# Kernel tuning notes

Hardware: AMD Instinct MI355X
Metric: run time of the kernel (lower is better)

## Reference

```python
import jax, jax.numpy as jnp
import numpy as np

B, T, D, E = 4, 2048, 1024, 8


def setup_inputs() -> dict:
    key = jax.random.key(0)
    ks = jax.random.split(key, 8)
    scale_g = float(np.sqrt(2.0 / (D + E)))  # xavier_uniform-ish scale for W_g
    scale_w = float(1.0 / np.sqrt(D))
    return {
        "x": jax.random.normal(ks[0], (B, T, D), dtype=jnp.float32),
        "noise": jax.random.normal(ks[1], (B, T, E), dtype=jnp.float32),  # the N(0,1) sample in Gating.forward
        "W_g": jax.random.normal(ks[2], (D, E), dtype=jnp.float32) * scale_g,
        "W_noise": jax.random.normal(ks[3], (D, E), dtype=jnp.float32),
        "W1": jax.random.normal(ks[4], (E, D, D), dtype=jnp.float32) * scale_w,
        "b1": jnp.zeros((E, D), dtype=jnp.float32),
        "W2": jax.random.normal(ks[5], (E, D, D), dtype=jnp.float32) * scale_w,
        "b2": jnp.zeros((E, D), dtype=jnp.float32),
        "k": 2,
    }


def _gates(x, noise, W_g, W_noise, k):
    # h = x@W_g + N(0,1) + softplus(x@W_noise)   (note: noise added, not scaled)
    h = jnp.einsum("btd,de->bte", x, W_g) + noise + jax.nn.softplus(
        jnp.einsum("btd,de->bte", x, W_noise)
    )
    kth = jax.lax.top_k(h, k)[0][..., -1:]           # kth largest per token
    h_masked = jnp.where(h >= kth, h, -jnp.inf)       # keepTopK (ties kept, as in torch)
    return jax.nn.softmax(h_masked, axis=-1)          # [B,T,E]


def reference(x, noise, W_g, W_noise, W1, b1, W2, b2, k):
    gates = _gates(x, noise, W_g, W_noise, k)
    # Dense loop over experts (faithful to original): every expert FFN on all tokens.
    # hidden: [E,B,T,D]
    hidden = jax.nn.relu(jnp.einsum("btd,edh->ebth", x, W1) + b1[:, None, None, :])
    expert_out = jnp.einsum("ebth,eho->ebto", hidden, W2) + b2[:, None, None, :]
    # mask-weighted combine: sum_e expert_out_e * gates[...,e]
    return jnp.einsum("ebtd,bte->btd", expert_out, gates)
```

## Files before the change

### kernel.cpp

```cpp
#include <hip/hip_runtime.h>
#include <hip/hip_bf16.h>

#define BTOK 8192
#define DDIM 1024
#define NEXP 8

typedef unsigned short u16;
typedef unsigned int u32;
typedef __attribute__((ext_vector_type(8))) short short8;
typedef __attribute__((ext_vector_type(4))) float f32x4;

constexpr int BM = 256, BN = 256, BK = 64;
constexpr int SLOTCAP = 3072;
constexpr int NT = DDIM / BK;

__device__ __forceinline__ u16 f2bf(float f){
  __hip_bfloat16 h = __float2bfloat16(f);
  return *reinterpret_cast<u16*>(&h);
}
__device__ __forceinline__ float bf2f(u16 v){
  return __uint_as_float(((u32)v) << 16);
}
__device__ __forceinline__ void gll16(const u16* gsrc, u16* ldst){
  __builtin_amdgcn_global_load_lds((const __attribute__((address_space(1))) void*)gsrc,
                                   (__attribute__((address_space(3))) void*)ldst,
                                   16, 0, 0);
}

#define GTOK 16
__global__ __launch_bounds__(512) void gating_score_kernel(
    const float* __restrict__ x, const float* __restrict__ noise,
    const float* __restrict__ Wg, const float* __restrict__ Wn,
    float* __restrict__ h_out, u16* __restrict__ xb)
{
  __shared__ float lw[2][NEXP][4][260];
  const int tid = threadIdx.x;

  for (int i = tid; i < 2*DDIM*NEXP; i += 512){
    const int mat = i >> 13;
    const int r   = i & 8191;
    const int d = r >> 3, ee = r & 7;
    const float* W = mat ? Wn : Wg;
    lw[mat][ee][d >> 8][d & 255] = W[r];
  }
  __syncthreads();

  const int q   = tid & 3;
  const int e   = (tid >> 2) & 7;
  const int tok = tid >> 5;
  const int t   = blockIdx.x * GTOK + tok;

  const float4* x4 = reinterpret_cast<const float4*>(x + (size_t)t*DDIM + q*256);
  const float4* g4 = reinterpret_cast<const float4*>(&lw[0][e][q][0]);
  const float4* n4 = reinterpret_cast<const float4*>(&lw[1][e][q][0]);
  ushort4* xb4 = reinterpret_cast<ushort4*>(xb + (size_t)t*DDIM + q*256);
  float agx=0.f, agz=0.f, anx=0.f, anz=0.f;
  #pragma unroll 8
  for (int j = 0; j < 64; ++j){
    const float4 xv = x4[j];
    const float4 wg = g4[j];
    const float4 wn = n4[j];
    agx = fmaf(xv.x,wg.x, fmaf(xv.y,wg.y, agx));
    agz = fmaf(xv.z,wg.z, fmaf(xv.w,wg.w, agz));
    anx = fmaf(xv.x,wn.x, fmaf(xv.y,wn.y, anx));
    anz = fmaf(xv.z,wn.z, fmaf(xv.w,wn.w, anz));
    if (e == 0)
      xb4[j] = make_ushort4(f2bf(xv.x), f2bf(xv.y), f2bf(xv.z), f2bf(xv.w));
  }
  float ag = agx + agz, an = anx + anz;
  ag += __shfl_xor(ag, 1); an += __shfl_xor(an, 1);
  ag += __shfl_xor(ag, 2); an += __shfl_xor(an, 2);
  if (q == 0){
    const float sp = (an > 20.f) ? an : log1pf(expf(an));
    h_out[(size_t)t*NEXP + e] = ag + noise[(size_t)t*NEXP + e] + sp;
  }
}

__global__ __launch_bounds__(256) void gating_select_kernel(
    const float* __restrict__ h_in, const int* __restrict__ kp,
    float* __restrict__ gates, int* __restrict__ counts, int* __restrict__ lists,
    int* __restrict__ tokmap, int* __restrict__ ncnt)
{
  __shared__ int lcnt[NEXP];
  __shared__ int lbase[NEXP];
  const int tid = threadIdx.x;
  const int t   = blockIdx.x*256 + tid;
  if (tid < NEXP) lcnt[tid] = 0;
  __syncthreads();

  float h[NEXP];
  const float4 h0 = reinterpret_cast<const float4*>(h_in + (size_t)t*NEXP)[0];
  const float4 h1 = reinterpret_cast<const float4*>(h_in + (size_t)t*NEXP)[1];
  h[0]=h0.x; h[1]=h0.y; h[2]=h0.z; h[3]=h0.w;
  h[4]=h1.x; h[5]=h1.y; h[6]=h1.z; h[7]=h1.w;

  int kk = *kp; kk = kk<1?1:(kk>NEXP?NEXP:kk);
  bool used[NEXP];
  #pragma unroll
  for (int e=0;e<NEXP;e++) used[e]=false;
  float kth = 0.f;
  for (int i=0;i<kk;i++){
    int bi=0; float bv=-3.4e38f;
    #pragma unroll
    for (int e=0;e<NEXP;e++) if (!used[e] && h[e]>bv){bv=h[e]; bi=e;}
    used[bi]=true; kth=bv;
  }
  float m=-3.4e38f;
  #pragma unroll
  for (int e=0;e<NEXP;e++) if (h[e]>=kth && h[e]>m) m=h[e];
  float p[NEXP], s=0.f;
  #pragma unroll
  for (int e=0;e<NEXP;e++){ p[e]=(h[e]>=kth)?expf(h[e]-m):0.f; s+=p[e]; }
  const float inv = 1.f/s;
  float g[NEXP];
  int lslot[NEXP];
  #pragma unroll
  for (int e=0;e<NEXP;e++){
    g[e] = p[e]*inv;
    gates[(size_t)t*NEXP + e] = g[e];
    if (g[e] > 0.f) lslot[e] = atomicAdd(&lcnt[e], 1);
  }
  __syncthreads();
  if (tid < NEXP) lbase[tid] = atomicAdd(&counts[tid], lcnt[tid]);
  __syncthreads();
  int idx = 0;
  #pragma unroll
  for (int e=0;e<NEXP;e++){
    if (g[e] > 0.f){
      const int slot = lbase[e] + lslot[e];
      lists[e*BTOK + slot] = t;
      tokmap[t*NEXP + idx] = (e << 13) | (slot & 8191);
      idx++;
    }
  }
  ncnt[t] = idx;
}

__global__ __launch_bounds__(256) void trans_kernel(
    const float* __restrict__ W1, const float* __restrict__ W2,
    u16* __restrict__ W1T, u16* __restrict__ W2T)
{
  __shared__ float tile[64][65];
  const int mz = blockIdx.z;
  const float* src = (mz < NEXP) ? (W1  + (size_t)mz*DDIM*DDIM) : (W2  + (size_t)(mz-NEXP)*DDIM*DDIM);
  u16*       dst = (mz < NEXP) ? (W1T + (size_t)mz*DDIM*DDIM) : (W2T + (size_t)(mz-NEXP)*DDIM*DDIM);
  const int r0 = blockIdx.x*64, c0 = blockIdx.y*64;
  const int tx = threadIdx.x & 63, ty = threadIdx.x >> 6;
  #pragma unroll
  for (int i=ty;i<64;i+=4)
    tile[i][tx] = src[(size_t)(r0+i)*DDIM + c0+tx];
  __syncthreads();
  #pragma unroll
  for (int i=ty;i<64;i+=4)
    dst[(size_t)(c0+i)*DDIM + r0+tx] = f2bf(tile[tx][i]);
}

template<int LAYER>
__device__ __forceinline__ void ffn_body(
    const u16* __restrict__ Asrc, const u16* __restrict__ WT,
    const float* __restrict__ bias,
    const int* __restrict__ counts, const int* __restrict__ lists,
    u16* __restrict__ dst)
{
  const int e  = blockIdx.z;
  int cnt = counts[e]; if (cnt > SLOTCAP) cnt = SLOTCAP;
  const int m0 = blockIdx.x*BM;
  if (m0 >= cnt) return;
  const int n0 = blockIdx.y*BN;

  __shared__ __align__(16) u16 ldsA[2][BM*BK];
  __shared__ __align__(16) u16 ldsB[2][BN*BK];

  const int tid = threadIdx.x;
  const int wave = tid>>6, lane = tid&63;
  const int wm = wave>>2, wn = wave&3;

  const u16* aSrc[4]; const u16* bSrc[4];
  {
    const int lr = lane>>3, sp = lane&7;
    #pragma unroll
    for (int i=0;i<4;i++){
      const int row = wave*32 + i*8 + lr;
      const int ku  = sp ^ (row&7);
      size_t abase;
      if constexpr (LAYER==1){
        int gr = m0 + row; if (gr >= cnt) gr = cnt-1;
        abase = (size_t)lists[e*BTOK + gr] * DDIM;
      } else {
        abase = ((size_t)e*SLOTCAP + m0 + row) * DDIM;
      }
      aSrc[i] = Asrc + abase + ku*8;
      bSrc[i] = WT + ((size_t)e*DDIM + n0 + row)*DDIM + ku*8;
    }
  }

  const int q = lane>>4, l16 = lane&15;
  int aoff[8], boff[4];
  #pragma unroll
  for (int f=0;f<8;f++){
    const int ra = wm*128 + f*16 + l16;
    aoff[f] = ra*BK + ((q ^ (ra&7))*8);
  }
  #pragma unroll
  for (int f=0;f<4;f++){
    const int rb = wn*64 + f*16 + l16;
    boff[f] = rb*BK + ((q ^ (rb&7))*8);
  }

  f32x4 acc[8][4];
  #pragma unroll
  for (int i=0;i<8;i++)
    #pragma unroll
    for (int j=0;j<4;j++)
      acc[i][j] = (f32x4){0.f,0.f,0.f,0.f};

  #define STAGE(T, c)                                            \
    _Pragma("unroll")                                            \
    for (int i=0;i<4;i++){                                       \
      gll16(aSrc[i] + (size_t)(T)*BK, &ldsA[c][(wave*32+i*8)*BK]); \
      gll16(bSrc[i] + (size_t)(T)*BK, &ldsB[c][(wave*32+i*8)*BK]); \
    }

  STAGE(0, 0)
  STAGE(1, 1)
  asm volatile("s_waitcnt vmcnt(8)" ::: "memory");
  __builtin_amdgcn_sched_barrier(0);
  __builtin_amdgcn_s_barrier();
  __builtin_amdgcn_sched_barrier(0);

  for (int kt = 0; kt < NT; ++kt){
    const int c = kt & 1;
    #pragma unroll
    for (int kk=0; kk<2; kk++){
      const int kx = kk ? 32 : 0;
      short8 bfr[4], afr[8];
      #pragma unroll
      for (int f=0;f<4;f++) bfr[f] = *reinterpret_cast<const short8*>(&ldsB[c][boff[f] ^ kx]);
      #pragma unroll
      for (int f=0;f<8;f++) afr[f] = *reinterpret_cast<const short8*>(&ldsA[c][aoff[f] ^ kx]);
      __builtin_amdgcn_s_setprio(1);
      #pragma unroll
      for (int fm=0;fm<8;fm++)
        #pragma unroll
        for (int fn=0;fn<4;fn++)
          acc[fm][fn] = __builtin_amdgcn_mfma_f32_16x16x32_bf16(afr[fm], bfr[fn], acc[fm][fn], 0, 0, 0);
      __builtin_amdgcn_s_setprio(0);
    }
    __builtin_amdgcn_sched_barrier(0);
    __builtin_amdgcn_s_barrier();
    __builtin_amdgcn_sched_barrier(0);
    if (kt + 2 < NT){
      STAGE(kt+2, c)
      asm volatile("s_waitcnt vmcnt(8)" ::: "memory");
    } else {
      asm volatile("s_waitcnt vmcnt(0)" ::: "memory");
    }
    __builtin_amdgcn_sched_barrier(0);
    __builtin_amdgcn_s_barrier();
    __builtin_amdgcn_sched_barrier(0);
  }
  #undef STAGE

  #pragma unroll
  for (int fm=0;fm<8;fm++){
    #pragma unroll
    for (int r=0;r<4;r++){
      const int row = wm*128 + fm*16 + q*4 + r;
      const int gr  = m0 + row;
      #pragma unroll
      for (int fn=0;fn<4;fn++){
        const int col = n0 + wn*64 + fn*16 + l16;
        float v = acc[fm][fn][r] + bias[e*DDIM + col];
        if constexpr (LAYER==1) v = v > 0.f ? v : 0.f;
        dst[((size_t)e*SLOTCAP + gr)*DDIM + col] = f2bf(v);
      }
    }
  }
}

__global__ __launch_bounds__(512, 2) void ffn1_kernel(
    const u16* __restrict__ A, const u16* __restrict__ WT, const float* __restrict__ b,
    const int* __restrict__ counts, const int* __restrict__ lists, u16* __restrict__ dst)
{ ffn_body<1>(A, WT, b, counts, lists, dst); }

__global__ __launch_bounds__(512, 2) void ffn2_kernel(
    const u16* __restrict__ A, const u16* __restrict__ WT, const float* __restrict__ b,
    const int* __restrict__ counts, const int* __restrict__ lists, u16* __restrict__ dst)
{ ffn_body<2>(A, WT, b, counts, lists, dst); }

__global__ __launch_bounds__(256) void combine_kernel(
    const u16* __restrict__ partial, const int* __restrict__ tokmap,
    const int* __restrict__ ncnt, const float* __restrict__ gates,
    float* __restrict__ out)
{
  const int t = blockIdx.x, c = threadIdx.x;
  const int n = ncnt[t];
  float4 acc = {0.f, 0.f, 0.f, 0.f};
  for (int j = 0; j < n; ++j){
    const int ent  = tokmap[t*NEXP + j];
    const int e    = ent >> 13, slot = ent & 8191;
    if (slot >= SLOTCAP) continue;
    const float g = gates[(size_t)t*NEXP + e];
    const ushort4 pv = reinterpret_cast<const ushort4*>(
        partial + ((size_t)e*SLOTCAP + slot)*DDIM)[c];
    acc.x = fmaf(g, bf2f(pv.x), acc.x);
    acc.y = fmaf(g, bf2f(pv.y), acc.y);
    acc.z = fmaf(g, bf2f(pv.z), acc.z);
    acc.w = fmaf(g, bf2f(pv.w), acc.w);
  }
  reinterpret_cast<float4*>(out + (size_t)t*DDIM)[c] = acc;
}

extern "C" void kernel_launch(void* const* d_in, const int* in_sizes, int n_in,
                              void* d_out, int out_size, void* d_ws, size_t ws_size,
                              hipStream_t stream)
{
  const float* x     = (const float*)d_in[0];
  const float* noise = (const float*)d_in[1];
  const float* Wg    = (const float*)d_in[2];
  const float* Wn    = (const float*)d_in[3];
  const float* W1    = (const float*)d_in[4];
  const float* b1    = (const float*)d_in[5];
  const float* W2    = (const float*)d_in[6];
  const float* b2    = (const float*)d_in[7];
  const int*   kp    = (const int*)d_in[8];
  float* out = (float*)d_out;

  char* ws = (char*)d_ws;
  int*   counts = (int*)ws;
  int*   lists  = (int*)(ws + 4096);
  float* gates  = (float*)(ws + 266240);
  int*   tokmap = (int*)(ws + 528384);
  int*   ncnt   = (int*)(ws + 790528);
  float* hbuf   = (float*)(ws + 823296);
  u16*   xb     = (u16*)(ws + 1085440);
  u16*   W1T    = (u16*)(ws + 17862656);
  u16*   W2T    = (u16*)(ws + 34639872);
  u16*   hidden = (u16*)(ws + 51417088);
  u16*   partial= (u16*)(ws + 101748736);
  const size_t NEED = 152080384ull;

  hipMemsetAsync(counts, 0, 64, stream);
  if (ws_size < NEED){
    hipMemsetAsync(d_out, 0, (size_t)out_size*sizeof(float), stream);
    return;
  }

  trans_kernel<<<dim3(16,16,16), 256, 0, stream>>>(W1, W2, W1T, W2T);
  gating_score_kernel<<<BTOK/GTOK, 512, 0, stream>>>(x, noise, Wg, Wn, hbuf, xb);
  gating_select_kernel<<<BTOK/256, 256, 0, stream>>>(hbuf, kp, gates, counts, lists,
                                                     tokmap, ncnt);
  ffn1_kernel<<<dim3(SLOTCAP/BM, DDIM/BN, NEXP), 512, 0, stream>>>(
      xb, W1T, b1, counts, lists, hidden);
  ffn2_kernel<<<dim3(SLOTCAP/BM, DDIM/BN, NEXP), 512, 0, stream>>>(
      hidden, W2T, b2, counts, lists, partial);
  combine_kernel<<<BTOK, 256, 0, stream>>>(partial, tokmap, ncnt, gates, out);
}
```

Baseline: 349.1 us.

## Move gating scores to split-bf16 MFMA and simplify FFN pipeline with smaller K tile

```diff
diff --git a/kernel.cpp b/kernel.cpp
--- a/kernel.cpp
+++ b/kernel.cpp
@@ -10,7 +10,7 @@
 typedef __attribute__((ext_vector_type(8))) short short8;
 typedef __attribute__((ext_vector_type(4))) float f32x4;
 
-constexpr int BM = 256, BN = 256, BK = 64;
+constexpr int BM = 256, BN = 256, BK = 32;
 constexpr int SLOTCAP = 3072;
 constexpr int NT = DDIM / BK;
 
@@ -27,57 +27,75 @@
                                    16, 0, 0);
 }
 
-#define GTOK 16
-__global__ __launch_bounds__(512) void gating_score_kernel(
-    const float* __restrict__ x, const float* __restrict__ noise,
+__global__ __launch_bounds__(256) void cast_x_kernel(const float4* __restrict__ x4,
+                                                     ushort4* __restrict__ xb4)
+{
+  const int i = blockIdx.x*256 + threadIdx.x;
+  const float4 v = x4[i];
+  xb4[i] = make_ushort4(f2bf(v.x), f2bf(v.y), f2bf(v.z), f2bf(v.w));
+}
+
+__global__ __launch_bounds__(256) void wprep_kernel(
     const float* __restrict__ Wg, const float* __restrict__ Wn,
-    float* __restrict__ h_out, u16* __restrict__ xb)
-{
-  __shared__ float lw[2][NEXP][4][260];
+    u16* __restrict__ wpt)
+{
+  const int idx = blockIdx.x*256 + threadIdx.x;
+  const int n = idx >> 10, d = idx & 1023;
+  const float v = (n < 8) ? Wg[d*8 + n] : Wn[d*8 + (n-8)];
+  const u16 hi = f2bf(v);
+  const u16 lo = f2bf(v - bf2f(hi));
+  wpt[n*1024 + d]          = hi;
+  wpt[16384 + n*1024 + d]  = lo;
+}
+
+__global__ __launch_bounds__(128) void score_kernel(
+    const float* __restrict__ x, const u16* __restrict__ xb,
+    const u16* __restrict__ wpt, float* __restrict__ hp)
+{
+  __shared__ __align__(16) u16 lw[2][16][1024];
   const int tid = threadIdx.x;
-
-  for (int i = tid; i < 2*DDIM*NEXP; i += 512){
-    const int mat = i >> 13;
-    const int r   = i & 8191;
-    const int d = r >> 3, ee = r & 7;
-    const float* W = mat ? Wn : Wg;
-    lw[mat][ee][d >> 8][d & 255] = W[r];
-  }
-  __syncthreads();
-
-  const int q   = tid & 3;
-  const int e   = (tid >> 2) & 7;
-  const int tok = tid >> 5;
-  const int t   = blockIdx.x * GTOK + tok;
-
-  const float4* x4 = reinterpret_cast<const float4*>(x + (size_t)t*DDIM + q*256);
-  const float4* g4 = reinterpret_cast<const float4*>(&lw[0][e][q][0]);
-  const float4* n4 = reinterpret_cast<const float4*>(&lw[1][e][q][0]);
-  ushort4* xb4 = reinterpret_cast<ushort4*>(xb + (size_t)t*DDIM + q*256);
-  float agx=0.f, agz=0.f, anx=0.f, anz=0.f;
-  #pragma unroll 8
-  for (int j = 0; j < 64; ++j){
-    const float4 xv = x4[j];
-    const float4 wg = g4[j];
-    const float4 wn = n4[j];
-    agx = fmaf(xv.x,wg.x, fmaf(xv.y,wg.y, agx));
-    agz = fmaf(xv.z,wg.z, fmaf(xv.w,wg.w, agz));
-    anx = fmaf(xv.x,wn.x, fmaf(xv.y,wn.y, anx));
-    anz = fmaf(xv.z,wn.z, fmaf(xv.w,wn.w, anz));
-    if (e == 0)
-      xb4[j] = make_ushort4(f2bf(xv.x), f2bf(xv.y), f2bf(xv.z), f2bf(xv.w));
-  }
-  float ag = agx + agz, an = anx + anz;
-  ag += __shfl_xor(ag, 1); an += __shfl_xor(an, 1);
-  ag += __shfl_xor(ag, 2); an += __shfl_xor(an, 2);
-  if (q == 0){
-    const float sp = (an > 20.f) ? an : log1pf(expf(an));
-    h_out[(size_t)t*NEXP + e] = ag + noise[(size_t)t*NEXP + e] + sp;
-  }
+  const int wave = tid >> 6, lane = tid & 63;
+
+  for (int it = 0; it < 32; ++it){
+    const int cid = it*128 + tid;
+    const int v = cid >> 11, rem = cid & 2047;
+    const int n = rem >> 7, c = rem & 127;
+    const short8 val = *reinterpret_cast<const short8*>(wpt + v*16384 + n*1024 + c*8);
+    *reinterpret_cast<short8*>(&lw[v][n][(c ^ (n&7))*8]) = val;
+  }
+  __syncthreads();
+
+  const int q = lane >> 4, l16 = lane & 15;
+  const int t0 = blockIdx.x*32 + wave*16;
+  const int rowA = t0 + l16;
+  const u16*   xbp = xb + (size_t)rowA*DDIM + q*8;
+  const float* xp  = x  + (size_t)rowA*DDIM + q*8;
+
+  f32x4 acc0 = {0.f,0.f,0.f,0.f}, acc1 = acc0, acc2 = acc0;
+  for (int kt = 0; kt < 32; ++kt){
+    const short8 ah = *reinterpret_cast<const short8*>(xbp + kt*32);
+    const float4 x0 = *reinterpret_cast<const float4*>(xp + kt*32);
+    const float4 x1 = *reinterpret_cast<const float4*>(xp + kt*32 + 4);
+    short8 al;
+    al[0]=(short)f2bf(x0.x - bf2f((u16)ah[0])); al[1]=(short)f2bf(x0.y - bf2f((u16)ah[1]));
+    al[2]=(short)f2bf(x0.z - bf2f((u16)ah[2])); al[3]=(short)f2bf(x0.w - bf2f((u16)ah[3]));
+    al[4]=(short)f2bf(x1.x - bf2f((u16)ah[4])); al[5]=(short)f2bf(x1.y - bf2f((u16)ah[5]));
+    al[6]=(short)f2bf(x1.z - bf2f((u16)ah[6])); al[7]=(short)f2bf(x1.w - bf2f((u16)ah[7]));
+    const int bs = ((kt*4 + q) ^ (l16 & 7)) * 8;
+    const short8 bh = *reinterpret_cast<const short8*>(&lw[0][l16][bs]);
+    const short8 bl = *reinterpret_cast<const short8*>(&lw[1][l16][bs]);
+    acc0 = __builtin_amdgcn_mfma_f32_16x16x32_bf16(ah, bh, acc0, 0, 0, 0);
+    acc1 = __builtin_amdgcn_mfma_f32_16x16x32_bf16(al, bh, acc1, 0, 0, 0);
+    acc2 = __builtin_amdgcn_mfma_f32_16x16x32_bf16(ah, bl, acc2, 0, 0, 0);
+  }
+  #pragma unroll
+  for (int r = 0; r < 4; ++r)
+    hp[(size_t)(t0 + q*4 + r)*16 + l16] = acc0[r] + acc1[r] + acc2[r];
 }
 
 __global__ __launch_bounds__(256) void gating_select_kernel(
-    const float* __restrict__ h_in, const int* __restrict__ kp,
+    const float* __restrict__ hp, const float* __restrict__ noise,
+    const int* __restrict__ kp,
     float* __restrict__ gates, int* __restrict__ counts, int* __restrict__ lists,
     int* __restrict__ tokmap, int* __restrict__ ncnt)
 {
@@ -88,11 +106,19 @@
   if (tid < NEXP) lcnt[tid] = 0;
   __syncthreads();
 
+  float hg[16];
+  #pragma unroll
+  for (int i = 0; i < 4; ++i){
+    const float4 v = reinterpret_cast<const float4*>(hp + (size_t)t*16)[i];
+    hg[i*4+0]=v.x; hg[i*4+1]=v.y; hg[i*4+2]=v.z; hg[i*4+3]=v.w;
+  }
   float h[NEXP];
-  const float4 h0 = reinterpret_cast<const float4*>(h_in + (size_t)t*NEXP)[0];
-  const float4 h1 = reinterpret_cast<const float4*>(h_in + (size_t)t*NEXP)[1];
-  h[0]=h0.x; h[1]=h0.y; h[2]=h0.z; h[3]=h0.w;
-  h[4]=h1.x; h[5]=h1.y; h[6]=h1.z; h[7]=h1.w;
+  #pragma unroll
+  for (int e = 0; e < NEXP; ++e){
+    const float hn = hg[8+e];
+    const float sp = (hn > 20.f) ? hn : log1pf(expf(hn));
+    h[e] = hg[e] + noise[(size_t)t*NEXP + e] + sp;
+  }
 
   int kk = *kp; kk = kk<1?1:(kk>NEXP?NEXP:kk);
   bool used[NEXP];
@@ -162,11 +188,13 @@
     const int* __restrict__ counts, const int* __restrict__ lists,
     u16* __restrict__ dst)
 {
-  const int e  = blockIdx.z;
+  const int lin = blockIdx.x;
+  const int e   = lin & 7;
+  const int idx = lin >> 3;
+  const int m0  = (idx >> 2) * BM;
+  const int n0  = (idx & 3)  * BN;
   int cnt = counts[e]; if (cnt > SLOTCAP) cnt = SLOTCAP;
-  const int m0 = blockIdx.x*BM;
   if (m0 >= cnt) return;
-  const int n0 = blockIdx.y*BN;
 
   __shared__ __align__(16) u16 ldsA[2][BM*BK];
   __shared__ __align__(16) u16 ldsB[2][BN*BK];
@@ -175,13 +203,13 @@
   const int wave = tid>>6, lane = tid&63;
   const int wm = wave>>2, wn = wave&3;
 
-  const u16* aSrc[4]; const u16* bSrc[4];
+  const u16* aSrc[2]; const u16* bSrc[2];
   {
-    const int lr = lane>>3, sp = lane&7;
+    const int lr = lane>>2, sp = lane&3;
     #pragma unroll
-    for (int i=0;i<4;i++){
-      const int row = wave*32 + i*8 + lr;
-      const int ku  = sp ^ (row&7);
+    for (int i=0;i<2;i++){
+      const int row = wave*32 + i*16 + lr;
+      const int ku  = sp ^ (row&3);
       size_t abase;
       if constexpr (LAYER==1){
         int gr = m0 + row; if (gr >= cnt) gr = cnt-1;
@@ -199,12 +227,12 @@
   #pragma unroll
   for (int f=0;f<8;f++){
     const int ra = wm*128 + f*16 + l16;
-    aoff[f] = ra*BK + ((q ^ (ra&7))*8);
+    aoff[f] = ra*BK + ((q ^ (ra&3))*8);
   }
   #pragma unroll
   for (int f=0;f<4;f++){
     const int rb = wn*64 + f*16 + l16;
-    boff[f] = rb*BK + ((q ^ (rb&7))*8);
+    boff[f] = rb*BK + ((q ^ (rb&3))*8);
   }
 
   f32x4 acc[8][4];
@@ -214,52 +242,38 @@
     for (int j=0;j<4;j++)
       acc[i][j] = (f32x4){0.f,0.f,0.f,0.f};
 
-  #define STAGE(T, c)                                            \
-    _Pragma("unroll")                                            \
-    for (int i=0;i<4;i++){                                       \
-      gll16(aSrc[i] + (size_t)(T)*BK, &ldsA[c][(wave*32+i*8)*BK]); \
-      gll16(bSrc[i] + (size_t)(T)*BK, &ldsB[c][(wave*32+i*8)*BK]); \
+  #define STAGE(T, c)                                               \
+    _Pragma("unroll")                                               \
+    for (int i=0;i<2;i++){                                          \
+      gll16(aSrc[i] + (size_t)(T)*BK, &ldsA[c][(wave*32+i*16)*BK]); \
+      gll16(bSrc[i] + (size_t)(T)*BK, &ldsB[c][(wave*32+i*16)*BK]); \
+    }
+  #define COMPUTE(c)                                                           \
+    {                                                                          \
+      short8 bfr[4], afr[8];                                                   \
+      _Pragma("unroll")                                                        \
+      for (int f=0;f<4;f++) bfr[f] = *reinterpret_cast<const short8*>(&ldsB[c][boff[f]]); \
+      _Pragma("unroll")                                                        \
+      for (int f=0;f<8;f++) afr[f] = *reinterpret_cast<const short8*>(&ldsA[c][aoff[f]]); \
+      _Pragma("unroll")                                                        \
+      for (int fm=0;fm<8;fm++)                                                 \
+        _Pragma("unroll")                                                      \
+        for (int fn=0;fn<4;fn++)                                               \
+          acc[fm][fn] = __builtin_amdgcn_mfma_f32_16x16x32_bf16(afr[fm], bfr[fn], acc[fm][fn], 0, 0, 0); \
     }
 
   STAGE(0, 0)
-  STAGE(1, 1)
-  asm volatile("s_waitcnt vmcnt(8)" ::: "memory");
-  __builtin_amdgcn_sched_barrier(0);
-  __builtin_amdgcn_s_barrier();
-  __builtin_amdgcn_sched_barrier(0);
-
-  for (int kt = 0; kt < NT; ++kt){
-    const int c = kt & 1;
-    #pragma unroll
-    for (int kk=0; kk<2; kk++){
-      const int kx = kk ? 32 : 0;
-      short8 bfr[4], afr[8];
-      #pragma unroll
-      for (int f=0;f<4;f++) bfr[f] = *reinterpret_cast<const short8*>(&ldsB[c][boff[f] ^ kx]);
-      #pragma unroll
-      for (int f=0;f<8;f++) afr[f] = *reinterpret_cast<const short8*>(&ldsA[c][aoff[f] ^ kx]);
-      __builtin_amdgcn_s_setprio(1);
-      #pragma unroll
-      for (int fm=0;fm<8;fm++)
-        #pragma unroll
-        for (int fn=0;fn<4;fn++)
-          acc[fm][fn] = __builtin_amdgcn_mfma_f32_16x16x32_bf16(afr[fm], bfr[fn], acc[fm][fn], 0, 0, 0);
-      __builtin_amdgcn_s_setprio(0);
-    }
-    __builtin_amdgcn_sched_barrier(0);
-    __builtin_amdgcn_s_barrier();
-    __builtin_amdgcn_sched_barrier(0);
-    if (kt + 2 < NT){
-      STAGE(kt+2, c)
-      asm volatile("s_waitcnt vmcnt(8)" ::: "memory");
-    } else {
-      asm volatile("s_waitcnt vmcnt(0)" ::: "memory");
-    }
-    __builtin_amdgcn_sched_barrier(0);
-    __builtin_amdgcn_s_barrier();
-    __builtin_amdgcn_sched_barrier(0);
-  }
+  __syncthreads();
+  int cur = 0;
+  for (int kt = 0; kt < NT-1; ++kt){
+    STAGE(kt+1, cur^1)
+    COMPUTE(cur)
+    __syncthreads();
+    cur ^= 1;
+  }
+  COMPUTE(cur)
   #undef STAGE
+  #undef COMPUTE
 
   #pragma unroll
   for (int fm=0;fm<8;fm++){
@@ -278,12 +292,12 @@
   }
 }
 
-__global__ __launch_bounds__(512, 2) void ffn1_kernel(
+__global__ __launch_bounds__(512, 4) void ffn1_kernel(
     const u16* __restrict__ A, const u16* __restrict__ WT, const float* __restrict__ b,
     const int* __restrict__ counts, const int* __restrict__ lists, u16* __restrict__ dst)
 { ffn_body<1>(A, WT, b, counts, lists, dst); }
 
-__global__ __launch_bounds__(512, 2) void ffn2_kernel(
+__global__ __launch_bounds__(512, 4) void ffn2_kernel(
     const u16* __restrict__ A, const u16* __restrict__ WT, const float* __restrict__ b,
     const int* __restrict__ counts, const int* __restrict__ lists, u16* __restrict__ dst)
 { ffn_body<2>(A, WT, b, counts, lists, dst); }
@@ -332,13 +346,14 @@
   float* gates  = (float*)(ws + 266240);
   int*   tokmap = (int*)(ws + 528384);
   int*   ncnt   = (int*)(ws + 790528);
-  float* hbuf   = (float*)(ws + 823296);
-  u16*   xb     = (u16*)(ws + 1085440);
-  u16*   W1T    = (u16*)(ws + 17862656);
-  u16*   W2T    = (u16*)(ws + 34639872);
-  u16*   hidden = (u16*)(ws + 51417088);
-  u16*   partial= (u16*)(ws + 101748736);
-  const size_t NEED = 152080384ull;
+  u16*   xb     = (u16*)(ws + 823296);
+  u16*   W1T    = (u16*)(ws + 17600512);
+  u16*   W2T    = (u16*)(ws + 34377728);
+  u16*   hidden = (u16*)(ws + 51154944);
+  u16*   partial= (u16*)(ws + 101486592);
+  float* hp     = (float*)(ws + 101486592);
+  u16*   wpt    = (u16*)(ws + 102010880);
+  const size_t NEED = 151818240ull;
 
   hipMemsetAsync(counts, 0, 64, stream);
   if (ws_size < NEED){
@@ -346,13 +361,15 @@
     return;
   }
 
+  cast_x_kernel<<<BTOK*DDIM/4/256, 256, 0, stream>>>((const float4*)x, (ushort4*)xb);
+  wprep_kernel<<<64, 256, 0, stream>>>(Wg, Wn, wpt);
   trans_kernel<<<dim3(16,16,16), 256, 0, stream>>>(W1, W2, W1T, W2T);
-  gating_score_kernel<<<BTOK/GTOK, 512, 0, stream>>>(x, noise, Wg, Wn, hbuf, xb);
-  gating_select_kernel<<<BTOK/256, 256, 0, stream>>>(hbuf, kp, gates, counts, lists,
+  score_kernel<<<BTOK/32, 128, 0, stream>>>(x, xb, wpt, hp);
+  gating_select_kernel<<<BTOK/256, 256, 0, stream>>>(hp, noise, kp, gates, counts, lists,
                                                      tokmap, ncnt);
-  ffn1_kernel<<<dim3(SLOTCAP/BM, DDIM/BN, NEXP), 512, 0, stream>>>(
+  ffn1_kernel<<<(SLOTCAP/BM)*4*NEXP, 512, 0, stream>>>(
       xb, W1T, b1, counts, lists, hidden);
-  ffn2_kernel<<<dim3(SLOTCAP/BM, DDIM/BN, NEXP), 512, 0, stream>>>(
+  ffn2_kernel<<<(SLOTCAP/BM)*4*NEXP, 512, 0, stream>>>(
       hidden, W2T, b2, counts, lists, partial);
   combine_kernel<<<BTOK, 256, 0, stream>>>(partial, tokmap, ncnt, gates, out);
 }
```

New measurement: 744.6 us. 113% more time.
